# Performance work log

Hardware: AMD Instinct MI355X
Metric: run time of the kernel (lower is better)

## Reference

```python
import jax, jax.numpy as jnp
import numpy as np

D_MODEL = 768
D_HEAD = 64
N_HEADS = D_MODEL // D_HEAD


def setup_inputs() -> dict:
    key = jax.random.key(0)
    k1, k2, k3 = jax.random.split(key, 3)
    n, h, w = 2, 48, 48
    x = jax.random.normal(k1, (n, h, w, D_MODEL), dtype=jnp.float32)
    # torch Linear weights: [out_features, in_features]
    w_qkv = jax.random.normal(k2, (3 * D_MODEL, D_MODEL), dtype=jnp.float32) * (D_MODEL ** -0.5)
    w_out = jax.random.normal(k3, (D_MODEL, D_MODEL), dtype=jnp.float32) * (D_MODEL ** -0.5)
    return {"x": x, "w_qkv": w_qkv, "w_out": w_out, "kernel_size": 7}


def _natten_mask(h: int, w: int, kernel_size: int) -> jnp.ndarray:
    # Faithful to _natten_mask_mod: q_x = idx // w, q_y = idx % w,
    # both axes compared against the same kernel_size.
    idx = jnp.arange(h * w)
    qx, qy = idx // w, idx % w
    horiz = jnp.abs(qx[:, None] - qx[None, :]) <= kernel_size
    vert = jnp.abs(qy[:, None] - qy[None, :]) <= kernel_size
    return horiz & vert  # [hw, hw] bool


def reference(x, w_qkv, w_out, kernel_size):
    n, h, w, d = x.shape
    hw = h * w
    qkv = jnp.einsum('nhwd,fd->nhwf', x, w_qkv)  # [n, h, w, 3*d]
    qkv = qkv.reshape(n, hw, 3, N_HEADS, D_HEAD)
    q = jnp.transpose(qkv[:, :, 0], (0, 2, 1, 3))  # [n, nh, hw, e]
    k = jnp.transpose(qkv[:, :, 1], (0, 2, 1, 3))
    v = jnp.transpose(qkv[:, :, 2], (0, 2, 1, 3))

    mask = _natten_mask(h, w, kernel_size)  # [hw, hw]
    scale = D_HEAD ** -0.5
    scores = jnp.einsum('bnqe,bnke->bnqk', q, k) * scale
    neg = jnp.asarray(jnp.finfo(scores.dtype).min, scores.dtype)
    scores = jnp.where(mask[None, None], scores, neg)
    attn = jax.nn.softmax(scores, axis=-1)
    o = jnp.einsum('bnqk,bnke->bnqe', attn, v)  # [n, nh, hw, e]
    o = jnp.transpose(o, (0, 2, 1, 3)).reshape(n, h, w, d)
    return jnp.einsum('nhwd,fd->nhwf', o, w_out)
```

## Files before the change

kernel.cpp:

```cpp
#include <hip/hip_runtime.h>

using f32x4 = __attribute__((ext_vector_type(4))) float;
using h8v   = __attribute__((ext_vector_type(8))) _Float16;
using h4v   = __attribute__((ext_vector_type(4))) _Float16;
using s8v   = __attribute__((ext_vector_type(8))) short;

#define MFMAH(a, b, c)   __builtin_amdgcn_mfma_f32_16x16x32_f16((a), (b), (c), 0, 0, 0)
#define MFMAH16(a, b, c) __builtin_amdgcn_mfma_f32_16x16x16f16((a), (b), (c), 0, 0, 0)

typedef __attribute__((address_space(3))) unsigned int lds_uint;
typedef const __attribute__((address_space(1))) unsigned int glb_uint;
__device__ inline void gload16(void* l, const void* g) {
    __builtin_amdgcn_global_load_lds((glb_uint*)g, (lds_uint*)l, 16, 0, 0);
}

__device__ inline float exp2_fast(float x) {
    float r;
    asm("v_exp_f32 %0, %1" : "=v"(r) : "v"(x));
    return r;
}

__global__ __launch_bounds__(256) void conv_all(const float* __restrict__ x,
                                                const float* __restrict__ wq,
                                                const float* __restrict__ wo,
                                                _Float16* __restrict__ xh,
                                                _Float16* __restrict__ wqh,
                                                _Float16* __restrict__ woh) {
    const int i = blockIdx.x * blockDim.x + threadIdx.x;
    const float* src;
    _Float16* dst;
    int off;
    if (i < 442368)      { src = x;  dst = xh;  off = i; }
    else if (i < 663552) { src = wq; dst = wqh; off = i - 442368; }
    else                 { src = wo; dst = woh; off = i - 663552; }
    const float4 a = *(const float4*)(src + (size_t)off * 8);
    const float4 b = *(const float4*)(src + (size_t)off * 8 + 4);
    h8v h;
    h[0] = (_Float16)a.x; h[1] = (_Float16)a.y; h[2] = (_Float16)a.z; h[3] = (_Float16)a.w;
    h[4] = (_Float16)b.x; h[5] = (_Float16)b.y; h[6] = (_Float16)b.z; h[7] = (_Float16)b.w;
    *(h8v*)(dst + (size_t)off * 8) = h;
}

__global__ __launch_bounds__(256) void gemm_qkv_f16(const _Float16* __restrict__ A,
                                                    const _Float16* __restrict__ B,
                                                    _Float16* __restrict__ C,
                                                    _Float16* __restrict__ vt) {
    constexpr int LD = 768, LDC = 2304;
    __shared__ __align__(16) _Float16 sA[128][64], sB[128][64];
    const int b = blockIdx.x;
    const int sb = (b & 7) * 81 + (b >> 3);
    const int bx = sb % 18, by = sb / 18;
    const int m0 = by * 128, n0 = bx * 128;
    const int tid = threadIdx.x, lane = tid & 63, wv = tid >> 6;
    const int wm = (wv >> 1) * 64, wn = (wv & 1) * 64;
    const int fr = lane & 15, fkb = (lane >> 4) * 8;

    const int srow = tid >> 3, scol = (tid & 7) * 8;
    const _Float16* gA = A + (size_t)(m0 + srow) * LD + scol;
    const _Float16* gB = B + (size_t)(n0 + srow) * LD + scol;

    f32x4 acc[4][4];
#pragma unroll
    for (int m = 0; m < 4; ++m)
#pragma unroll
        for (int n2 = 0; n2 < 4; ++n2) acc[m][n2] = (f32x4){0.f, 0.f, 0.f, 0.f};

    for (int kt = 0; kt < 12; ++kt) {
        const int k0 = kt * 64;
#pragma unroll
        for (int q = 0; q < 4; ++q) {
            gload16(&sA[q * 32 + srow][scol], gA + (size_t)(q * 32) * LD + k0);
            gload16(&sB[q * 32 + srow][scol], gB + (size_t)(q * 32) * LD + k0);
        }
        __syncthreads();

#pragma unroll
        for (int kk = 0; kk < 2; ++kk) {
            h8v fa[4], fb[4];
#pragma unroll
            for (int m = 0; m < 4; ++m) fa[m] = *(const h8v*)&sA[wm + m * 16 + fr][kk * 32 + fkb];
#pragma unroll
            for (int n2 = 0; n2 < 4; ++n2) fb[n2] = *(const h8v*)&sB[wn + n2 * 16 + fr][kk * 32 + fkb];
#pragma unroll
            for (int m = 0; m < 4; ++m)
#pragma unroll
                for (int n2 = 0; n2 < 4; ++n2) acc[m][n2] = MFMAH(fa[m], fb[n2], acc[m][n2]);
        }
        __syncthreads();
    }

    const int rg = (lane >> 4) * 4;
    if (bx < 12) {
#pragma unroll
        for (int m = 0; m < 4; ++m)
#pragma unroll
            for (int n2 = 0; n2 < 4; ++n2)
#pragma unroll
                for (int r = 0; r < 4; ++r)
                    C[(size_t)(m0 + wm + m * 16 + rg + r) * LDC + (n0 + wn + n2 * 16 + fr)] =
                        (_Float16)acc[m][n2][r];
    } else {
        const int nb = m0 / 2304;
        const int tokb = m0 - nb * 2304 + wm + rg;
#pragma unroll
        for (int m = 0; m < 4; ++m)
#pragma unroll
            for (int n2 = 0; n2 < 4; ++n2) {
                const int f = n0 - 1536 + wn + n2 * 16 + fr;
                const int head = f >> 6, e = f & 63;
                h4v v;
#pragma unroll
                for (int r = 0; r < 4; ++r) v[r] = (_Float16)acc[m][n2][r];
                *(h4v*)(vt + (size_t)((nb * 12 + head) * 64 + e) * 2304 + tokb + m * 16) = v;
            }
    }
}

__global__ __launch_bounds__(192) void attn_flash(const _Float16* __restrict__ qkv,
                                                  const _Float16* __restrict__ vt,
                                                  _Float16* __restrict__ o,
                                                  const int* __restrict__ ksp) {
    __shared__ __align__(16) char sbuf[2][14336];
    const int tid = threadIdx.x;
    const int lane = tid & 63, wv = tid >> 6;
    const int fr = lane & 15, fg = lane >> 4;

    const int b = blockIdx.x;
    const int xcd = b & 7, g = b >> 3;
    const int qx = xcd * 6 + g / 24;
    const int hn = g % 24;
    const int head = hn >> 1, n = hn & 1;
    const int KS = *ksp;

    const int krow0 = tid >> 3, kc = tid & 7;
    const int vrow0 = tid / 6,  vc = tid % 6;
    const int ksw = (krow0 & 7) << 4;
    const int vsw = (vrow0 & 7) << 4;

    const int qy = wv * 16 + fr;
    const _Float16* qrow = qkv + (size_t)(n * 2304 + qx * 48 + qy) * 2304 + head * 64;
    h8v qa0 = *(const h8v*)(qrow + fg * 8);
    h8v qa1 = *(const h8v*)(qrow + 32 + fg * 8);
    qa0 = qa0 * (_Float16)0.1803368801f;
    qa1 = qa1 * (_Float16)0.1803368801f;

    int nt0 = (wv * 16 - KS) >> 4;      if (nt0 < 0) nt0 = 0;
    int nt1 = (wv * 16 + 15 + KS) >> 4; if (nt1 > 2) nt1 = 2;

    f32x4 mbias[3];
#pragma unroll
    for (int nt = 0; nt < 3; ++nt)
#pragma unroll
        for (int r = 0; r < 4; ++r) {
            const int dy = nt * 16 + fg * 4 + r - qy;
            mbias[nt][r] = (dy < -KS || dy > KS) ? -1e4f : 0.f;
        }

    f32x4 Oacc[4];
#pragma unroll
    for (int e = 0; e < 4; ++e) Oacc[e] = (f32x4){0.f, 0.f, 0.f, 0.f};
    float rs_acc = 0.f;

    const int lo = (qx - KS) > 0 ? (qx - KS) : 0;
    const int hi = (qx + KS) < 47 ? (qx + KS) : 47;

    const _Float16* kgbase = qkv + (size_t)(n * 2304) * 2304 + 768 + head * 64;
    const _Float16* vgbase = vt + (size_t)((n * 12 + head) * 64) * 2304;

    {
        const _Float16* kg = kgbase + (size_t)(lo * 48) * 2304;
        const _Float16* vg = vgbase + lo * 48;
        const s8v a0 = *(const s8v*)(kg + (size_t)krow0 * 2304 + kc * 8);
        const s8v a1 = *(const s8v*)(kg + (size_t)(krow0 + 24) * 2304 + kc * 8);
        const s8v b0 = *(const s8v*)(vg + (size_t)vrow0 * 2304 + vc * 8);
        const s8v b1 = *(const s8v*)(vg + (size_t)(vrow0 + 32) * 2304 + vc * 8);
        *(s8v*)(sbuf[0] + krow0 * 128 + ((kc * 16) ^ ksw)) = a0;
        *(s8v*)(sbuf[0] + (krow0 + 24) * 128 + ((kc * 16) ^ ksw)) = a1;
        *(s8v*)(sbuf[0] + 6144 + vrow0 * 128 + ((vc * 16) ^ vsw)) = b0;
        *(s8v*)(sbuf[0] + 6144 + (vrow0 + 32) * 128 + ((vc * 16) ^ vsw)) = b1;
    }

    int p = 0;
    for (int kx = lo; kx <= hi; ++kx) {
        __syncthreads();
        const bool pre = (kx < hi);
        s8v tk0, tk1, tv0, tv1;
        if (pre) {
            const _Float16* kg = kgbase + (size_t)((kx + 1) * 48) * 2304;
            const _Float16* vg = vgbase + (kx + 1) * 48;
            tk0 = *(const s8v*)(kg + (size_t)krow0 * 2304 + kc * 8);
            tk1 = *(const s8v*)(kg + (size_t)(krow0 + 24) * 2304 + kc * 8);
            tv0 = *(const s8v*)(vg + (size_t)vrow0 * 2304 + vc * 8);
            tv1 = *(const s8v*)(vg + (size_t)(vrow0 + 32) * 2304 + vc * 8);
        }

        const char* K = sbuf[p];
        const char* V = sbuf[p] + 6144;
        __builtin_amdgcn_s_setprio(1);

        f32x4 s[3];
#pragma unroll
        for (int nt = 0; nt < 3; ++nt)
            if (nt >= nt0 && nt <= nt1) {
                const int rr = nt * 16 + fr;
                const int sw = (rr & 7) << 4;
                const h8v kb0 = *(const h8v*)(K + rr * 128 + ((fg * 16) ^ sw));
                const h8v kb1 = *(const h8v*)(K + rr * 128 + ((64 + fg * 16) ^ sw));
                f32x4 z = MFMAH(kb0, qa0, mbias[nt]);
                z = MFMAH(kb1, qa1, z);
                s[nt] = z;
            }

#pragma unroll
        for (int nt = 0; nt < 3; ++nt)
            if (nt >= nt0 && nt <= nt1) {
                h4v pa;
#pragma unroll
                for (int r = 0; r < 4; ++r) {
                    const float pv = exp2_fast(s[nt][r]);
                    rs_acc += pv;
                    pa[r] = (_Float16)pv;
                }
                const int slot = nt * 2 + (fg >> 1), off8 = (fg & 1) * 8;
#pragma unroll
                for (int et = 0; et < 4; ++et) {
                    const int rv = et * 16 + fr;
                    const h4v vb = *(const h4v*)(V + rv * 128 +
                                                 (((slot ^ (rv & 7)) << 4) + off8));
                    Oacc[et] = MFMAH16(vb, pa, Oacc[et]);
                }
            }
        __builtin_amdgcn_s_setprio(0);

        if (pre) {
            char* d = sbuf[p ^ 1];
            *(s8v*)(d + krow0 * 128 + ((kc * 16) ^ ksw)) = tk0;
            *(s8v*)(d + (krow0 + 24) * 128 + ((kc * 16) ^ ksw)) = tk1;
            *(s8v*)(d + 6144 + vrow0 * 128 + ((vc * 16) ^ vsw)) = tv0;
            *(s8v*)(d + 6144 + (vrow0 + 32) * 128 + ((vc * 16) ^ vsw)) = tv1;
        }
        p ^= 1;
    }

    rs_acc += __shfl_xor(rs_acc, 16);
    rs_acc += __shfl_xor(rs_acc, 32);
    const float linv = 1.f / rs_acc;
    _Float16* ob = o + (size_t)(n * 2304 + qx * 48 + wv * 16 + fr) * 768 + head * 64;
#pragma unroll
    for (int et = 0; et < 4; ++et) {
        h4v ov;
#pragma unroll
        for (int r = 0; r < 4; ++r) ov[r] = (_Float16)(Oacc[et][r] * linv);
        *(h4v*)(ob + et * 16 + fg * 4) = ov;
    }
}

__global__ __launch_bounds__(256) void gemm_out_f16(const _Float16* __restrict__ A,
                                                    const _Float16* __restrict__ B,
                                                    float* __restrict__ C) {
    constexpr int LD = 768, LDC = 768;
    __shared__ __align__(16) _Float16 sA[128][64], sB[128][64];
    const int b = blockIdx.x;
    const int sb = (b & 7) * 27 + (b >> 3);
    const int bx = sb % 6, by = sb / 6;
    const int m0 = by * 128, n0 = bx * 128;
    const int tid = threadIdx.x, lane = tid & 63, wv = tid >> 6;
    const int wm = (wv >> 1) * 64, wn = (wv & 1) * 64;
    const int fr = lane & 15, fkb = (lane >> 4) * 8;

    const int srow = tid >> 3, scol = (tid & 7) * 8;
    const _Float16* gA = A + (size_t)(m0 + srow) * LD + scol;
    const _Float16* gB = B + (size_t)(n0 + srow) * LD + scol;

    f32x4 acc[4][4];
#pragma unroll
    for (int m = 0; m < 4; ++m)
#pragma unroll
        for (int n2 = 0; n2 < 4; ++n2) acc[m][n2] = (f32x4){0.f, 0.f, 0.f, 0.f};

    for (int kt = 0; kt < 12; ++kt) {
        const int k0 = kt * 64;
#pragma unroll
        for (int q = 0; q < 4; ++q) {
            gload16(&sA[q * 32 + srow][scol], gA + (size_t)(q * 32) * LD + k0);
            gload16(&sB[q * 32 + srow][scol], gB + (size_t)(q * 32) * LD + k0);
        }
        __syncthreads();

#pragma unroll
        for (int kk = 0; kk < 2; ++kk) {
            h8v fa[4], fb[4];
#pragma unroll
            for (int m = 0; m < 4; ++m) fa[m] = *(const h8v*)&sA[wm + m * 16 + fr][kk * 32 + fkb];
#pragma unroll
            for (int n2 = 0; n2 < 4; ++n2) fb[n2] = *(const h8v*)&sB[wn + n2 * 16 + fr][kk * 32 + fkb];
#pragma unroll
            for (int m = 0; m < 4; ++m)
#pragma unroll
                for (int n2 = 0; n2 < 4; ++n2) acc[m][n2] = MFMAH(fa[m], fb[n2], acc[m][n2]);
        }
        __syncthreads();
    }

    const int rg = (lane >> 4) * 4;
#pragma unroll
    for (int m = 0; m < 4; ++m)
#pragma unroll
        for (int n2 = 0; n2 < 4; ++n2)
#pragma unroll
            for (int r = 0; r < 4; ++r)
                C[(size_t)(m0 + wm + m * 16 + rg + r) * LDC + (n0 + wn + n2 * 16 + fr)] =
                    acc[m][n2][r];
}

extern "C" void kernel_launch(void* const* d_in, const int* in_sizes, int n_in,
                              void* d_out, int out_size, void* d_ws, size_t ws_size,
                              hipStream_t stream) {
    const float* x     = (const float*)d_in[0];
    const float* w_qkv = (const float*)d_in[1];
    const float* w_out = (const float*)d_in[2];
    const int*   ksp   = (const int*)d_in[3];
    float* out = (float*)d_out;

    char* ws = (char*)d_ws;
    _Float16* qkv = (_Float16*)(ws);
    _Float16* vt  = (_Float16*)(ws + 21237760);
    _Float16* o   = (_Float16*)(ws + 28315648);
    _Float16* xh  = (_Float16*)(ws + 35393536);
    _Float16* wqh = (_Float16*)(ws + 42471424);
    _Float16* woh = (_Float16*)(ws + 46010368);

    conv_all<<<dim3(2880), 256, 0, stream>>>(x, w_qkv, w_out, xh, wqh, woh);
    gemm_qkv_f16<<<dim3(648), 256, 0, stream>>>(xh, wqh, qkv, vt);
    attn_flash<<<dim3(1152), 192, 0, stream>>>(qkv, vt, o, ksp);
    gemm_out_f16<<<dim3(216), 256, 0, stream>>>(o, woh, out);
}
```

Baseline: 82.45 us.

## Double-buffer LDS tiles in QKV and output GEMMs with K=32 stages

Both GEMM kernels now split K into 32-wide stages held in two LDS buffers, issuing the next stage's global-to-LDS loads before computing on the current one. This is meant to overlap global memory latency with MFMA work and drops the second barrier per iteration. The trade-off is twice as many loop iterations and barriers, a full vmcnt(0) wait each step, and less MFMA work per stage to hide latency.

New measurement: 88.11 us. +6.9%, slower.

```diff
diff --git a/kernel.cpp b/kernel.cpp
--- a/kernel.cpp
+++ b/kernel.cpp
@@ -46,7 +46,7 @@
                                                     _Float16* __restrict__ C,
                                                     _Float16* __restrict__ vt) {
     constexpr int LD = 768, LDC = 2304;
-    __shared__ __align__(16) _Float16 sA[128][64], sB[128][64];
+    __shared__ __align__(16) _Float16 sA[2][128][32], sB[2][128][32];
     const int b = blockIdx.x;
     const int sb = (b & 7) * 81 + (b >> 3);
     const int bx = sb % 18, by = sb / 18;
@@ -55,7 +55,7 @@
     const int wm = (wv >> 1) * 64, wn = (wv & 1) * 64;
     const int fr = lane & 15, fkb = (lane >> 4) * 8;
 
-    const int srow = tid >> 3, scol = (tid & 7) * 8;
+    const int srow = tid >> 2, scol = (tid & 3) * 8;
     const _Float16* gA = A + (size_t)(m0 + srow) * LD + scol;
     const _Float16* gB = B + (size_t)(n0 + srow) * LD + scol;
 
@@ -65,28 +65,33 @@
 #pragma unroll
         for (int n2 = 0; n2 < 4; ++n2) acc[m][n2] = (f32x4){0.f, 0.f, 0.f, 0.f};
 
-    for (int kt = 0; kt < 12; ++kt) {
-        const int k0 = kt * 64;
-#pragma unroll
-        for (int q = 0; q < 4; ++q) {
-            gload16(&sA[q * 32 + srow][scol], gA + (size_t)(q * 32) * LD + k0);
-            gload16(&sB[q * 32 + srow][scol], gB + (size_t)(q * 32) * LD + k0);
-        }
+    gload16(&sA[0][srow][scol],      gA);
+    gload16(&sA[0][64 + srow][scol], gA + 64 * LD);
+    gload16(&sB[0][srow][scol],      gB);
+    gload16(&sB[0][64 + srow][scol], gB + 64 * LD);
+
+    int cur = 0;
+    for (int kt = 0; kt < 24; ++kt) {
+        asm volatile("s_waitcnt vmcnt(0)" ::: "memory");
         __syncthreads();
-
-#pragma unroll
-        for (int kk = 0; kk < 2; ++kk) {
-            h8v fa[4], fb[4];
-#pragma unroll
-            for (int m = 0; m < 4; ++m) fa[m] = *(const h8v*)&sA[wm + m * 16 + fr][kk * 32 + fkb];
-#pragma unroll
-            for (int n2 = 0; n2 < 4; ++n2) fb[n2] = *(const h8v*)&sB[wn + n2 * 16 + fr][kk * 32 + fkb];
-#pragma unroll
-            for (int m = 0; m < 4; ++m)
-#pragma unroll
-                for (int n2 = 0; n2 < 4; ++n2) acc[m][n2] = MFMAH(fa[m], fb[n2], acc[m][n2]);
-        }
-        __syncthreads();
+        if (kt + 1 < 24) {
+            const int k1 = (kt + 1) * 32;
+            gload16(&sA[cur ^ 1][srow][scol],      gA + k1);
+            gload16(&sA[cur ^ 1][64 + srow][scol], gA + 64 * LD + k1);
+            gload16(&sB[cur ^ 1][srow][scol],      gB + k1);
+            gload16(&sB[cur ^ 1][64 + srow][scol], gB + 64 * LD + k1);
+        }
+
+        h8v fa[4], fb[4];
+#pragma unroll
+        for (int m = 0; m < 4; ++m) fa[m] = *(const h8v*)&sA[cur][wm + m * 16 + fr][fkb];
+#pragma unroll
+        for (int n2 = 0; n2 < 4; ++n2) fb[n2] = *(const h8v*)&sB[cur][wn + n2 * 16 + fr][fkb];
+#pragma unroll
+        for (int m = 0; m < 4; ++m)
+#pragma unroll
+            for (int n2 = 0; n2 < 4; ++n2) acc[m][n2] = MFMAH(fa[m], fb[n2], acc[m][n2]);
+        cur ^= 1;
     }
 
     const int rg = (lane >> 4) * 4;
@@ -259,7 +264,7 @@
                                                     const _Float16* __restrict__ B,
                                                     float* __restrict__ C) {
     constexpr int LD = 768, LDC = 768;
-    __shared__ __align__(16) _Float16 sA[128][64], sB[128][64];
+    __shared__ __align__(16) _Float16 sA[2][128][32], sB[2][128][32];
     const int b = blockIdx.x;
     const int sb = (b & 7) * 27 + (b >> 3);
     const int bx = sb % 6, by = sb / 6;
@@ -268,7 +273,7 @@
     const int wm = (wv >> 1) * 64, wn = (wv & 1) * 64;
     const int fr = lane & 15, fkb = (lane >> 4) * 8;
 
-    const int srow = tid >> 3, scol = (tid & 7) * 8;
+    const int srow = tid >> 2, scol = (tid & 3) * 8;
     const _Float16* gA = A + (size_t)(m0 + srow) * LD + scol;
     const _Float16* gB = B + (size_t)(n0 + srow) * LD + scol;
 
@@ -278,28 +283,33 @@
 #pragma unroll
         for (int n2 = 0; n2 < 4; ++n2) acc[m][n2] = (f32x4){0.f, 0.f, 0.f, 0.f};
 
-    for (int kt = 0; kt < 12; ++kt) {
-        const int k0 = kt * 64;
-#pragma unroll
-        for (int q = 0; q < 4; ++q) {
-            gload16(&sA[q * 32 + srow][scol], gA + (size_t)(q * 32) * LD + k0);
-            gload16(&sB[q * 32 + srow][scol], gB + (size_t)(q * 32) * LD + k0);
-        }
+    gload16(&sA[0][srow][scol],      gA);
+    gload16(&sA[0][64 + srow][scol], gA + 64 * LD);
+    gload16(&sB[0][srow][scol],      gB);
+    gload16(&sB[0][64 + srow][scol], gB + 64 * LD);
+
+    int cur = 0;
+    for (int kt = 0; kt < 24; ++kt) {
+        asm volatile("s_waitcnt vmcnt(0)" ::: "memory");
         __syncthreads();
-
-#pragma unroll
-        for (int kk = 0; kk < 2; ++kk) {
-            h8v fa[4], fb[4];
-#pragma unroll
-            for (int m = 0; m < 4; ++m) fa[m] = *(const h8v*)&sA[wm + m * 16 + fr][kk * 32 + fkb];
-#pragma unroll
-            for (int n2 = 0; n2 < 4; ++n2) fb[n2] = *(const h8v*)&sB[wn + n2 * 16 + fr][kk * 32 + fkb];
-#pragma unroll
-            for (int m = 0; m < 4; ++m)
-#pragma unroll
-                for (int n2 = 0; n2 < 4; ++n2) acc[m][n2] = MFMAH(fa[m], fb[n2], acc[m][n2]);
-        }
-        __syncthreads();
+        if (kt + 1 < 24) {
+            const int k1 = (kt + 1) * 32;
+            gload16(&sA[cur ^ 1][srow][scol],      gA + k1);
+            gload16(&sA[cur ^ 1][64 + srow][scol], gA + 64 * LD + k1);
+            gload16(&sB[cur ^ 1][srow][scol],      gB + k1);
+            gload16(&sB[cur ^ 1][64 + srow][scol], gB + 64 * LD + k1);
+        }
+
+        h8v fa[4], fb[4];
+#pragma unroll
+        for (int m = 0; m < 4; ++m) fa[m] = *(const h8v*)&sA[cur][wm + m * 16 + fr][fkb];
+#pragma unroll
+        for (int n2 = 0; n2 < 4; ++n2) fb[n2] = *(const h8v*)&sB[cur][wn + n2 * 16 + fr][fkb];
+#pragma unroll
+        for (int m = 0; m < 4; ++m)
+#pragma unroll
+            for (int n2 = 0; n2 < 4; ++n2) acc[m][n2] = MFMAH(fa[m], fb[n2], acc[m][n2]);
+        cur ^= 1;
     }
 
     const int rg = (lane >> 4) * 4;
```
